# Kernel tuning notes

Hardware: AMD Instinct MI355X
Metric: run time of the kernel (lower is better)

Reference implementation:

```python
import jax, jax.numpy as jnp
import numpy as np

S, B, HID, NH = 256, 2, 512, 8
HD = HID // NH
C = 1.0            # Poincare ball curvature c (geoopt k = -c)
SQC = C ** 0.5
EPS = 1e-15


def _artanh(x):
    return jnp.arctanh(jnp.clip(x, -1 + 1e-7, 1 - 1e-7))


def artan_k(x):
    return _artanh(SQC * x) / SQC


def tan_k(x):
    return jnp.tanh(SQC * x) / SQC


def mobius_add(x, y):
    x2 = jnp.sum(x * x, -1, keepdims=True)
    y2 = jnp.sum(y * y, -1, keepdims=True)
    xy = jnp.sum(x * y, -1, keepdims=True)
    num = (1 + 2 * C * xy + C * y2) * x + (1 - C * x2) * y
    den = 1 + 2 * C * xy + C * C * x2 * y2
    return num / jnp.maximum(den, EPS)


def mobius_matvec(W, x):
    x_norm = jnp.maximum(jnp.linalg.norm(x, axis=-1, keepdims=True), EPS)
    mx = x @ W.T
    mx_norm = jnp.maximum(jnp.linalg.norm(mx, axis=-1, keepdims=True), EPS)
    res = tan_k(mx_norm / x_norm * artan_k(x_norm)) * (mx / mx_norm)
    zero = jnp.all(mx == 0, axis=-1, keepdims=True)
    return jnp.where(zero, 0.0, res)


def projx(x):
    n = jnp.maximum(jnp.linalg.norm(x, axis=-1, keepdims=True), EPS)
    maxnorm = (1 - 4e-3) / SQC  # float32 eps in geoopt
    return jnp.where(n > maxnorm, x / n * maxnorm, x)


def expmap0(u):
    n = jnp.maximum(jnp.linalg.norm(u, axis=-1, keepdims=True), EPS)
    return tan_k(n) * u / n


def logmap0(y):
    n = jnp.maximum(jnp.linalg.norm(y, axis=-1, keepdims=True), EPS)
    return artan_k(n) * y / n


def mobius_scalar_mul(r, x):
    n = jnp.maximum(jnp.linalg.norm(x, axis=-1, keepdims=True), EPS)
    return tan_k(r * artan_k(n)) * x / n


def manifold_linear(W, b, x):
    return projx(mobius_add(mobius_matvec(W, x), b))


def setup_inputs() -> dict:
    key = jax.random.key(0)
    ks = jax.random.split(key, 7)
    q = jax.random.normal(ks[0], (S, B, HID), jnp.float32) * 0.02
    w = lambda k: jax.random.normal(k, (HID, HID), jnp.float32) * 0.02
    bias = lambda k: jax.random.normal(k, (HID,), jnp.float32) * 0.01
    return {"query": q,
            "Wq": w(ks[1]), "bq": bias(ks[2]),
            "Wk": w(ks[3]), "bk": bias(ks[4]),
            "Wv": w(ks[5]), "bv": bias(ks[6])}


def reference(query, Wq, bq, Wk, bk, Wv, bv):
    x = jnp.transpose(query, (1, 0, 2))  # [B,S,HID], key=value=query
    Bn, Sn, _ = x.shape
    q = manifold_linear(Wq, bq, x)
    k = manifold_linear(Wk, bk, x)
    v = manifold_linear(Wv, bv, x)
    # faithful to torch .view(-1, H, S, D): plain memory reshape (not transpose)
    ql = expmap0(logmap0(q).reshape(Bn, NH, Sn, HD))
    kl = expmap0(logmap0(k).reshape(Bn, NH, Sn, HD))
    vl = expmap0(logmap0(v).reshape(Bn, NH, Sn, HD))
    # pairwise mobius_add(-q, k) -> [B,H,Q,N,D]; torch norm(p=-2) over D (faithful)
    diff = mobius_add(-ql[:, :, :, None, :], kl[:, :, None, :, :])
    t1 = jnp.sum(jnp.maximum(diff * diff, 1e-30) ** -1.0, axis=-1) ** -0.5
    scores = jnp.clip(-2.0 * artan_k(t1), -1e10, 1e10)
    probs = jax.nn.sigmoid(scores)  # [B,H,Q,N]; dropout p=0 -> identity
    # weighted gyro-midpoint over N (geoopt _weighted_midpoint, reducedim=[-1])
    gamma = 2.0 / jnp.maximum(1.0 - C * jnp.sum(vl * vl, -1), EPS)  # [B,H,N]
    denom = jnp.einsum('bhqn,bhn->bhq', probs, gamma - 1.0)
    sgn = jnp.where(denom >= 0, 1.0, -1.0)
    denom = sgn * jnp.maximum(jnp.abs(denom), 1e-10)
    nom = jnp.einsum('bhqn,bhnd->bhqd', probs, gamma[..., None] * vl)
    ctx = mobius_scalar_mul(0.5, nom / denom[..., None])  # [B,H,Q,D]
    ctx = jnp.transpose(ctx, (0, 2, 1, 3))  # [B,Q,H,D]
    ctx = expmap0(logmap0(ctx).reshape(Bn, Sn, HID))
    return jnp.transpose(ctx, (1, 0, 2)), probs
```

## Files before the change

### kernel.cpp

```cpp
#include <hip/hip_runtime.h>
#include <math.h>

constexpr int S_   = 256;
constexpr int B_   = 2;
constexpr int HID_ = 512;
constexpr int NH_  = 8;
constexpr int HD_  = 64;
constexpr int BSH  = B_ * S_ * HID_;

typedef unsigned short u16;
typedef short s16x8 __attribute__((ext_vector_type(8)));
typedef float f32x4 __attribute__((ext_vector_type(4)));

__device__ __forceinline__ float artanh_c(float x) {
    x = fminf(fmaxf(x, -0.9999999f), 0.9999999f);
    return 0.5f * __logf((1.f + x) / (1.f - x));
}

__device__ __forceinline__ float wsum64(float v) {
    #pragma unroll
    for (int o = 1; o < 64; o <<= 1) v += __shfl_xor(v, o, 64);
    return v;
}

__device__ __forceinline__ float block_sum_256(float v, float* red) {
    const int t = threadIdx.x;
    __syncthreads();
    red[t] = v;
    __syncthreads();
    #pragma unroll
    for (int sft = 128; sft > 0; sft >>= 1) {
        if (t < sft) red[t] += red[t + sft];
        __syncthreads();
    }
    return red[0];
}

__device__ __forceinline__ void split8(const float* v, s16x8& hi, s16x8& lo) {
    #pragma unroll
    for (int j = 0; j < 8; ++j) {
        const unsigned u = __float_as_uint(v[j]);
        const float hf = __uint_as_float(u & 0xFFFF0000u);
        hi[j] = (short)(u >> 16);
        lo[j] = (short)(__float_as_uint(v[j] - hf) >> 16);
    }
}

__global__ __launch_bounds__(256) void gemm3_fused_kernel(
    const float* __restrict__ query,
    const float* __restrict__ Wq, const float* __restrict__ Wk,
    const float* __restrict__ Wv, float* __restrict__ ws_mx)
{
    const int tid = threadIdx.x;
    const int rt = blockIdx.x >> 3;
    const int ct = blockIdx.x & 7;
    const int which = (rt * 32) >> 9;
    const int rloc  = (rt * 32) & 511;
    const float* __restrict__ W = (which == 0) ? Wq : (which == 1) ? Wk : Wv;

    __shared__ __align__(16) u16 sA[2][2][32 * 64];
    __shared__ __align__(16) u16 sB[2][2][64 * 64];

    const int ra = tid >> 3, sa = tid & 7;
    const int rb = tid >> 2, hb = (tid & 3) * 2;
    const int axrow = rloc + ra;
    const float* gA = query + (size_t)((axrow & 255) * 2 + (axrow >> 8)) * HID_ + sa * 8;
    const float* gB = W + (size_t)(ct * 64 + rb) * HID_ + hb * 8;
    const int wA  = ra * 64 + ((sa ^ (ra & 7)) * 8);
    const int wB0 = rb * 64 + ((hb ^ (rb & 7)) * 8);
    const int wB1 = rb * 64 + (((hb + 1) ^ (rb & 7)) * 8);

    const int lane = tid & 63, wv = tid >> 6;
    const int fr = lane & 15, fs = lane >> 4;
    const int aB0 = fr * 64,        ax0 = fr & 7;
    const int aB1 = (16 + fr) * 64, ax1 = (16 + fr) & 7;
    const int bB  = (wv * 16 + fr) * 64, bx = (wv * 16 + fr) & 7;

    float a8[8], b16[16];
    f32x4 acc[2] = {(f32x4){0.f,0.f,0.f,0.f}, (f32x4){0.f,0.f,0.f,0.f}};

#define G3_LOAD(c)  do { \
        const int k0 = (c) * 64; \
        *(float4*)&a8[0]  = *(const float4*)(gA + k0); \
        *(float4*)&a8[4]  = *(const float4*)(gA + k0 + 4); \
        *(float4*)&b16[0] = *(const float4*)(gB + k0); \
        *(float4*)&b16[4] = *(const float4*)(gB + k0 + 4); \
        *(float4*)&b16[8] = *(const float4*)(gB + k0 + 8); \
        *(float4*)&b16[12]= *(const float4*)(gB + k0 + 12); \
    } while (0)

#define G3_WRITE(b) do { \
        s16x8 h_, l_; \
        split8(a8, h_, l_); \
        *(s16x8*)&sA[b][0][wA] = h_;  *(s16x8*)&sA[b][1][wA] = l_; \
        split8(&b16[0], h_, l_); \
        *(s16x8*)&sB[b][0][wB0] = h_; *(s16x8*)&sB[b][1][wB0] = l_; \
        split8(&b16[8], h_, l_); \
        *(s16x8*)&sB[b][0][wB1] = h_; *(s16x8*)&sB[b][1][wB1] = l_; \
    } while (0)

    G3_LOAD(0);
    G3_WRITE(0);

    for (int c = 0; c < 8; ++c) {
        const int p = c & 1;
        __syncthreads();
        if (c < 7) G3_LOAD(c + 1);
        #pragma unroll
        for (int h = 0; h < 2; ++h) {
            const int sl = h * 4 + fs;
            s16x8 ah0 = *(const s16x8*)&sA[p][0][aB0 + ((sl ^ ax0) * 8)];
            s16x8 al0 = *(const s16x8*)&sA[p][1][aB0 + ((sl ^ ax0) * 8)];
            s16x8 ah1 = *(const s16x8*)&sA[p][0][aB1 + ((sl ^ ax1) * 8)];
            s16x8 al1 = *(const s16x8*)&sA[p][1][aB1 + ((sl ^ ax1) * 8)];
            s16x8 bh  = *(const s16x8*)&sB[p][0][bB  + ((sl ^ bx)  * 8)];
            s16x8 bl  = *(const s16x8*)&sB[p][1][bB  + ((sl ^ bx)  * 8)];
            acc[0] = __builtin_amdgcn_mfma_f32_16x16x32_bf16(ah0, bh, acc[0], 0, 0, 0);
            acc[0] = __builtin_amdgcn_mfma_f32_16x16x32_bf16(ah0, bl, acc[0], 0, 0, 0);
            acc[0] = __builtin_amdgcn_mfma_f32_16x16x32_bf16(al0, bh, acc[0], 0, 0, 0);
            acc[1] = __builtin_amdgcn_mfma_f32_16x16x32_bf16(ah1, bh, acc[1], 0, 0, 0);
            acc[1] = __builtin_amdgcn_mfma_f32_16x16x32_bf16(ah1, bl, acc[1], 0, 0, 0);
            acc[1] = __builtin_amdgcn_mfma_f32_16x16x32_bf16(al1, bh, acc[1], 0, 0, 0);
        }
        if (c < 7) G3_WRITE((c + 1) & 1);
    }
#undef G3_LOAD
#undef G3_WRITE

    #pragma unroll
    for (int i = 0; i < 2; ++i)
        #pragma unroll
        for (int q = 0; q < 4; ++q)
            ws_mx[(size_t)(rt * 32 + i * 16 + fs * 4 + q) * HID_ + ct * 64 + wv * 16 + fr]
                = acc[i][q];
}

__global__ __launch_bounds__(256) void mobius_rows_kernel(
    const float* __restrict__ query,
    const float* __restrict__ bq, const float* __restrict__ bk,
    const float* __restrict__ bv,
    float* __restrict__ ws_qkv, float* __restrict__ ws_gamma)
{
    const int lane = threadIdx.x & 63;
    const int wv   = threadIdx.x >> 6;
    const int row  = blockIdx.x * 4 + wv;
    const int which = row >> 9;
    const int rr    = row & 511;
    const float* __restrict__ bias = (which == 0) ? bq : (which == 1) ? bk : bv;
    float* mrow = ws_qkv + (size_t)row * HID_;
    const float* xrow = query + (size_t)((rr & 255) * 2 + (rr >> 8)) * HID_;

    float m[8], x[8], bb[8];
    *(float4*)&m[0]  = ((const float4*)mrow)[lane * 2];
    *(float4*)&m[4]  = ((const float4*)mrow)[lane * 2 + 1];
    *(float4*)&x[0]  = ((const float4*)xrow)[lane * 2];
    *(float4*)&x[4]  = ((const float4*)xrow)[lane * 2 + 1];
    *(float4*)&bb[0] = ((const float4*)bias)[lane * 2];
    *(float4*)&bb[4] = ((const float4*)bias)[lane * 2 + 1];

    float x2p = 0.f, m2p = 0.f, b2p = 0.f;
    #pragma unroll
    for (int j = 0; j < 8; ++j) {
        x2p = fmaf(x[j], x[j], x2p);
        m2p = fmaf(m[j], m[j], m2p);
        b2p = fmaf(bb[j], bb[j], b2p);
    }
    const float x2s = wsum64(x2p);
    const float mn2 = wsum64(m2p);
    const float b2s = wsum64(b2p);
    const float xn = fmaxf(sqrtf(x2s), 1e-15f);
    const float mn = fmaxf(sqrtf(mn2), 1e-15f);
    const float fac = tanhf(mn / xn * artanh_c(xn)) / mn;
    float r[8];
    float r2p = 0.f, ryp = 0.f;
    #pragma unroll
    for (int j = 0; j < 8; ++j) {
        r[j] = fac * m[j];
        r2p = fmaf(r[j], r[j], r2p);
        ryp = fmaf(r[j], bb[j], ryp);
    }
    const float r2s = wsum64(r2p);
    const float ry  = wsum64(ryp);
    const float a_c = 1.f + 2.f * ry + b2s;
    const float b_c = 1.f - r2s;
    const float den = 1.f + 2.f * ry + r2s * b2s;
    const float inv_den = 1.f / fmaxf(den, 1e-15f);
    float h[8];
    float h2p = 0.f;
    #pragma unroll
    for (int j = 0; j < 8; ++j) {
        h[j] = (a_c * r[j] + b_c * bb[j]) * inv_den;
        h2p = fmaf(h[j], h[j], h2p);
    }
    const float h2s = wsum64(h2p);
    float hn = fmaxf(sqrtf(h2s), 1e-15f);
    float pf = 1.f;
    if (hn > 0.996f) { pf = 0.996f / hn; hn = 0.996f; }
    const float lf = artanh_c(hn) / hn * pf;
    float l[8];
    float l2p = 0.f;
    #pragma unroll
    for (int j = 0; j < 8; ++j) {
        l[j] = lf * h[j];
        l2p = fmaf(l[j], l[j], l2p);
    }
    float cs = l2p;
    cs += __shfl_xor(cs, 1, 64);
    cs += __shfl_xor(cs, 2, 64);
    cs += __shfl_xor(cs, 4, 64);
    const float cn = fmaxf(sqrtf(cs), 1e-15f);
    const float th = tanhf(cn);
    const float sc = th / cn;
    float o[8];
    #pragma unroll
    for (int j = 0; j < 8; ++j) o[j] = sc * l[j];
    ((float4*)mrow)[lane * 2]     = *(float4*)&o[0];
    ((float4*)mrow)[lane * 2 + 1] = *(float4*)&o[4];
    if (which == 2 && (lane & 7) == 0) {
        const int j = lane >> 3;
        ws_gamma[(size_t)rr * NH_ + j] = 2.f / fmaxf(1.f - th * th, 1e-15f);
    }
}

__global__ __launch_bounds__(256) void attn_kernel(
    const float* __restrict__ ws_qkv, const float* __restrict__ gamma,
    float* __restrict__ probs, float* __restrict__ lc)
{
    const int tid = threadIdx.x;
    const int bh  = blockIdx.x >> 5;
    const int q0  = (blockIdx.x & 31) * 8;
    const float* __restrict__ ql = ws_qkv + (size_t)bh * (S_ * HD_);
    const float* __restrict__ kl = ws_qkv + (size_t)BSH + (size_t)bh * (S_ * HD_);
    const float* __restrict__ vl = ws_qkv + (size_t)2 * BSH + (size_t)bh * (S_ * HD_);

    __shared__ __align__(16) float kS[128 * 64];
    __shared__ __align__(16) float qS[8 * 64];
    __shared__ __align__(16) float pS[8 * 256];
    __shared__ float gS[S_];
    __shared__ float k2S[128];
    __shared__ float nomP[4][8][64];
    __shared__ float dnS[8];

    gS[tid] = gamma[(size_t)bh * S_ + tid];
    if (tid < 128) ((float4*)qS)[tid] = ((const float4*)(ql + (size_t)q0 * 64))[tid];
    __syncthreads();

    const int q_l = tid >> 5;
    const int n_i = tid & 31;
    float qv[64];
    #pragma unroll
    for (int c = 0; c < 16; ++c)
        *(float4*)&qv[c * 4] = *(const float4*)&qS[q_l * 64 + c * 4];
    float q2 = 0.f;
    #pragma unroll
    for (int d = 0; d < 64; ++d) q2 = fmaf(qv[d], qv[d], q2);
    const float b_c = 1.f - q2;
    float* __restrict__ prow = probs + ((size_t)(bh * S_ + q0 + q_l)) * S_;

    const int c4 = tid & 15;
    const int nb = tid >> 4;
    float sp = 0.f, spg = 0.f;

    for (int half = 0; half < 2; ++half) {
        __syncthreads();
        #pragma unroll
        for (int jj = 0; jj < 8; ++jj) {
            const int n = nb + 16 * jj;
            const float4 v = *(const float4*)(kl + ((size_t)(half * 128 + n)) * 64 + c4 * 4);
            *(float4*)&kS[n * 64 + ((c4 ^ (n & 15)) * 4)] = v;
            float pk = fmaf(v.x, v.x, fmaf(v.y, v.y, fmaf(v.z, v.z, v.w * v.w)));
            pk += __shfl_xor(pk, 1, 64);
            pk += __shfl_xor(pk, 2, 64);
            pk += __shfl_xor(pk, 4, 64);
            pk += __shfl_xor(pk, 8, 64);
            if (c4 == 0) k2S[n] = pk;
        }
        __syncthreads();
        #pragma unroll
        for (int j = 0; j < 4; ++j) {
            const int n = n_i + 32 * j;
            float kv[64];
            #pragma unroll
            for (int c = 0; c < 16; ++c)
                *(float4*)&kv[c * 4] = *(const float4*)&kS[n * 64 + ((c ^ (n & 15)) * 4)];
            float s = 0.f;
            #pragma unroll
            for (int d = 0; d < 64; ++d) s = fmaf(qv[d], kv[d], s);
            const float k2  = k2S[n];
            const float a_c = 1.f - 2.f * s + k2;
            const float den = fmaxf(fmaf(q2, k2, 1.f - 2.f * s), 1e-15f);
            const float ra  = __builtin_amdgcn_rcpf(a_c);
            const float r_c = b_c * ra;
            const float scale = den * den * ra * ra;
            const float c2  = 1e-30f * scale;
            float invsum = 0.f;
            #pragma unroll
            for (int d = 0; d < 64; ++d) {
                const float w = fmaf(r_c, kv[d], -qv[d]);
                invsum += __builtin_amdgcn_rcpf(fmaf(w, w, c2));
            }
            const float t1 = __builtin_amdgcn_rsqf(scale * invsum);
            const float p = 0.5f - 0.5f * fminf(t1, 0.9999999f);
            const int gn = half * 128 + n;
            prow[gn] = p;
            const float g = gS[gn];
            pS[q_l * 256 + gn] = p * g;
            sp += p; spg += p * g;
        }
    }
    #pragma unroll
    for (int o = 1; o < 32; o <<= 1) {
        sp  += __shfl_xor(sp, o, 64);
        spg += __shfl_xor(spg, o, 64);
    }
    if ((tid & 31) == 0) dnS[q_l] = spg - sp;
    __syncthreads();

    const int w = tid >> 6, d = tid & 63;
    float acc[8] = {};
    const float* __restrict__ vbase = vl + (size_t)(w * 64) * 64;
    #pragma unroll 4
    for (int i4 = 0; i4 < 16; ++i4) {
        float vv[4];
        #pragma unroll
        for (int j2 = 0; j2 < 4; ++j2) vv[j2] = vbase[(size_t)(i4 * 4 + j2) * 64 + d];
        #pragma unroll
        for (int qq = 0; qq < 8; ++qq) {
            const float4 pq = *(const float4*)&pS[qq * 256 + w * 64 + i4 * 4];
            acc[qq] = fmaf(pq.x, vv[0], acc[qq]);
            acc[qq] = fmaf(pq.y, vv[1], acc[qq]);
            acc[qq] = fmaf(pq.z, vv[2], acc[qq]);
            acc[qq] = fmaf(pq.w, vv[3], acc[qq]);
        }
    }
    #pragma unroll
    for (int qq = 0; qq < 8; ++qq) nomP[w][qq][d] = acc[qq];
    __syncthreads();

    #pragma unroll
    for (int t = 0; t < 2; ++t) {
        const int qq = (tid >> 6) + 4 * t;
        const float nom = nomP[0][qq][d] + nomP[1][qq][d] + nomP[2][qq][d] + nomP[3][qq][d];
        const float dd = dnS[qq];
        const float adn = fmaxf(fabsf(dd), 1e-10f);
        const float sden = (dd >= 0.f) ? adn : -adn;
        const float m = nom / sden;
        const float ss = wsum64(m * m);
        const float nn = fmaxf(sqrtf(ss), 1e-15f);
        const float s1 = tanhf(0.5f * artanh_c(nn));
        const float res = s1 * m / nn;
        const float nres = fmaxf(s1, 1e-15f);
        lc[((size_t)(bh * S_ + q0 + qq)) * HD_ + d] = (artanh_c(nres) / nres) * res;
    }
}

__global__ __launch_bounds__(256) void outproj_kernel(
    const float* __restrict__ lc, float* __restrict__ out0)
{
    const int t = threadIdx.x;
    const int s = blockIdx.x & (S_ - 1);
    const int b = blockIdx.x >> 8;
    __shared__ float red[256];
    const int h0 = t >> 6, d0 = t & 63;
    const int e1 = t + 256;
    const int h1 = e1 >> 6, d1 = e1 & 63;
    const float v0 = lc[(((size_t)(b * NH_ + h0)) * S_ + s) * HD_ + d0];
    const float v1 = lc[(((size_t)(b * NH_ + h1)) * S_ + s) * HD_ + d1];
    const float ss = block_sum_256(v0 * v0 + v1 * v1, red);
    const float nn = fmaxf(sqrtf(ss), 1e-15f);
    const float f = tanhf(nn) / nn;
    float* orow = out0 + ((size_t)(s * B_ + b)) * HID_;
    orow[t] = f * v0;
    orow[t + 256] = f * v1;
}

extern "C" void kernel_launch(void* const* d_in, const int* in_sizes, int n_in,
                              void* d_out, int out_size, void* d_ws, size_t ws_size,
                              hipStream_t stream) {
    (void)in_sizes; (void)n_in; (void)out_size; (void)ws_size;
    const float* query = (const float*)d_in[0];
    const float* Wq = (const float*)d_in[1];
    const float* bq = (const float*)d_in[2];
    const float* Wk = (const float*)d_in[3];
    const float* bk = (const float*)d_in[4];
    const float* Wv = (const float*)d_in[5];
    const float* bv = (const float*)d_in[6];

    float* out0  = (float*)d_out;
    float* probs = out0 + (size_t)S_ * B_ * HID_;

    float* ws       = (float*)d_ws;
    float* ws_qkv   = ws;
    float* ws_gamma = ws + (size_t)3 * BSH;
    float* ws_lc    = ws + (size_t)3 * BSH + 4096;

    gemm3_fused_kernel<<<dim3(384), dim3(256), 0, stream>>>(query, Wq, Wk, Wv, ws_qkv);
    mobius_rows_kernel<<<dim3(384), dim3(256), 0, stream>>>(query, bq, bk, bv, ws_qkv, ws_gamma);
    attn_kernel<<<dim3(512), dim3(256), 0, stream>>>(ws_qkv, ws_gamma, probs, ws_lc);
    outproj_kernel<<<dim3(B_ * S_), dim3(256), 0, stream>>>(ws_lc, out0);
}
```

Measured before the change: 108.8 us.

## Split attention head dimension across two half-waves with 512-thread blocks

Doubles the attention kernel's block to 512 threads and has each query's 64 lanes split the 64-wide head dimension into two 32-element halves, combining partial dot products and reciprocal sums with a cross-half shuffle. This halves per-thread register arrays (qv/kv) so more waves can be resident and the latency-bound per-pair work is spread over more threads. The PV accumulation is re-partitioned over 8 warps of 32 keys each, and the nomP reduction grows to 8 partials. It adds extra shuffles and leaves half the lanes idle for the store and probability-accumulation step.

```diff
diff --git a/kernel.cpp b/kernel.cpp
--- a/kernel.cpp
+++ b/kernel.cpp
@@ -7,6 +7,7 @@
 constexpr int NH_  = 8;
 constexpr int HD_  = 64;
 constexpr int BSH  = B_ * S_ * HID_;
+
 
 typedef unsigned short u16;
 typedef short s16x8 __attribute__((ext_vector_type(8)));
@@ -222,7 +223,7 @@
     }
 }
 
-__global__ __launch_bounds__(256) void attn_kernel(
+__global__ __launch_bounds__(512, 4) void attn_kernel(
     const float* __restrict__ ws_qkv, const float* __restrict__ gamma,
     float* __restrict__ probs, float* __restrict__ lc)
 {
@@ -238,22 +239,27 @@
     __shared__ __align__(16) float pS[8 * 256];
     __shared__ float gS[S_];
     __shared__ float k2S[128];
-    __shared__ float nomP[4][8][64];
+    __shared__ float nomP[8][8][64];
     __shared__ float dnS[8];
 
-    gS[tid] = gamma[(size_t)bh * S_ + tid];
+    if (tid < 256) gS[tid] = gamma[(size_t)bh * S_ + tid];
     if (tid < 128) ((float4*)qS)[tid] = ((const float4*)(ql + (size_t)q0 * 64))[tid];
     __syncthreads();
 
-    const int q_l = tid >> 5;
-    const int n_i = tid & 31;
-    float qv[64];
-    #pragma unroll
-    for (int c = 0; c < 16; ++c)
-        *(float4*)&qv[c * 4] = *(const float4*)&qS[q_l * 64 + c * 4];
-    float q2 = 0.f;
-    #pragma unroll
-    for (int d = 0; d < 64; ++d) q2 = fmaf(qv[d], qv[d], q2);
+    const int lane = tid & 63;
+    const int q_l  = tid >> 6;
+    const int n_i  = lane & 31;
+    const int dh   = lane >> 5;
+    const int d0   = dh * 32;
+
+    float qv[32];
+    #pragma unroll
+    for (int c = 0; c < 8; ++c)
+        *(float4*)&qv[c * 4] = *(const float4*)&qS[q_l * 64 + d0 + c * 4];
+    float q2p = 0.f;
+    #pragma unroll
+    for (int d = 0; d < 32; ++d) q2p = fmaf(qv[d], qv[d], q2p);
+    const float q2 = q2p + __shfl_xor(q2p, 32, 64);
     const float b_c = 1.f - q2;
     float* __restrict__ prow = probs + ((size_t)(bh * S_ + q0 + q_l)) * S_;
 
@@ -264,8 +270,8 @@
     for (int half = 0; half < 2; ++half) {
         __syncthreads();
         #pragma unroll
-        for (int jj = 0; jj < 8; ++jj) {
-            const int n = nb + 16 * jj;
+        for (int jj = 0; jj < 4; ++jj) {
+            const int n = nb + 32 * jj;
             const float4 v = *(const float4*)(kl + ((size_t)(half * 128 + n)) * 64 + c4 * 4);
             *(float4*)&kS[n * 64 + ((c4 ^ (n & 15)) * 4)] = v;
             float pk = fmaf(v.x, v.x, fmaf(v.y, v.y, fmaf(v.z, v.z, v.w * v.w)));
@@ -279,13 +285,20 @@
         #pragma unroll
         for (int j = 0; j < 4; ++j) {
             const int n = n_i + 32 * j;
-            float kv[64];
+            float kv[32];
             #pragma unroll
-            for (int c = 0; c < 16; ++c)
-                *(float4*)&kv[c * 4] = *(const float4*)&kS[n * 64 + ((c ^ (n & 15)) * 4)];
-            float s = 0.f;
+            for (int c = 0; c < 8; ++c) {
+                const int sl = dh * 8 + c;
+                *(float4*)&kv[c * 4] = *(const float4*)&kS[n * 64 + ((sl ^ (n & 15)) * 4)];
+            }
+            float s0 = 0.f, s1 = 0.f;
             #pragma unroll
-            for (int d = 0; d < 64; ++d) s = fmaf(qv[d], kv[d], s);
+            for (int d = 0; d < 32; d += 2) {
+                s0 = fmaf(qv[d],     kv[d],     s0);
+                s1 = fmaf(qv[d + 1], kv[d + 1], s1);
+            }
+            float s = s0 + s1;
+            s += __shfl_xor(s, 32, 64);
             const float k2  = k2S[n];
             const float a_c = 1.f - 2.f * s + k2;
             const float den = fmaxf(fmaf(q2, k2, 1.f - 2.f * s), 1e-15f);
@@ -293,40 +306,43 @@
             const float r_c = b_c * ra;
             const float scale = den * den * ra * ra;
             const float c2  = 1e-30f * scale;
-            float invsum = 0.f;
+            float is0 = 0.f, is1 = 0.f;
             #pragma unroll
-            for (int d = 0; d < 64; ++d) {
-                const float w = fmaf(r_c, kv[d], -qv[d]);
-                invsum += __builtin_amdgcn_rcpf(fmaf(w, w, c2));
+            for (int d = 0; d < 32; d += 2) {
+                const float w0 = fmaf(r_c, kv[d],     -qv[d]);
+                const float w1 = fmaf(r_c, kv[d + 1], -qv[d + 1]);
+                is0 += __builtin_amdgcn_rcpf(fmaf(w0, w0, c2));
+                is1 += __builtin_amdgcn_rcpf(fmaf(w1, w1, c2));
             }
+            float invsum = is0 + is1;
+            invsum += __shfl_xor(invsum, 32, 64);
             const float t1 = __builtin_amdgcn_rsqf(scale * invsum);
             const float p = 0.5f - 0.5f * fminf(t1, 0.9999999f);
             const int gn = half * 128 + n;
-            prow[gn] = p;
-            const float g = gS[gn];
-            pS[q_l * 256 + gn] = p * g;
-            sp += p; spg += p * g;
+            if (dh == 0) {
+                prow[gn] = p;
+                const float g = gS[gn];
+                pS[q_l * 256 + gn] = p * g;
+                sp += p; spg += p * g;
+            }
         }
     }
-    #pragma unroll
-    for (int o = 1; o < 32; o <<= 1) {
-        sp  += __shfl_xor(sp, o, 64);
-        spg += __shfl_xor(spg, o, 64);
-    }
-    if ((tid & 31) == 0) dnS[q_l] = spg - sp;
+    sp  = wsum64(sp);
+    spg = wsum64(spg);
+    if (lane == 0) dnS[q_l] = spg - sp;
     __syncthreads();
 
-    const int w = tid >> 6, d = tid & 63;
+    const int w = q_l, d = lane;
     float acc[8] = {};
-    const float* __restrict__ vbase = vl + (size_t)(w * 64) * 64;
-    #pragma unroll 4
-    for (int i4 = 0; i4 < 16; ++i4) {
+    const float* __restrict__ vbase = vl + (size_t)(w * 32) * 64;
+    #pragma unroll
+    for (int i4 = 0; i4 < 8; ++i4) {
         float vv[4];
         #pragma unroll
         for (int j2 = 0; j2 < 4; ++j2) vv[j2] = vbase[(size_t)(i4 * 4 + j2) * 64 + d];
         #pragma unroll
         for (int qq = 0; qq < 8; ++qq) {
-            const float4 pq = *(const float4*)&pS[qq * 256 + w * 64 + i4 * 4];
+            const float4 pq = *(const float4*)&pS[qq * 256 + w * 32 + i4 * 4];
             acc[qq] = fmaf(pq.x, vv[0], acc[qq]);
             acc[qq] = fmaf(pq.y, vv[1], acc[qq]);
             acc[qq] = fmaf(pq.z, vv[2], acc[qq]);
@@ -337,10 +353,11 @@
     for (int qq = 0; qq < 8; ++qq) nomP[w][qq][d] = acc[qq];
     __syncthreads();
 
-    #pragma unroll
-    for (int t = 0; t < 2; ++t) {
-        const int qq = (tid >> 6) + 4 * t;
-        const float nom = nomP[0][qq][d] + nomP[1][qq][d] + nomP[2][qq][d] + nomP[3][qq][d];
+    {
+        const int qq = q_l;
+        float nom = 0.f;
+        #pragma unroll
+        for (int w2 = 0; w2 < 8; ++w2) nom += nomP[w2][qq][d];
         const float dd = dnS[qq];
         const float adn = fmaxf(fabsf(dd), 1e-10f);
         const float sden = (dd >= 0.f) ? adn : -adn;
@@ -396,6 +413,6 @@
 
     gemm3_fused_kernel<<<dim3(384), dim3(256), 0, stream>>>(query, Wq, Wk, Wv, ws_qkv);
     mobius_rows_kernel<<<dim3(384), dim3(256), 0, stream>>>(query, bq, bk, bv, ws_qkv, ws_gamma);
-    attn_kernel<<<dim3(512), dim3(256), 0, stream>>>(ws_qkv, ws_gamma, probs, ws_lc);
+    attn_kernel<<<dim3(512), dim3(512), 0, stream>>>(ws_qkv, ws_gamma, probs, ws_lc);
     outproj_kernel<<<dim3(B_ * S_), dim3(256), 0, stream>>>(ws_lc, out0);
 }
```

Measured after the change: 106.6 us. 2.0% less time.

## Restructure attention: one key per thread, 4 queries per block, more blocks

Applied to the files above, without the earlier changes.

The attention kernel now assigns one key row per thread, held in registers and read directly from global memory, and loops over 4 queries per block. This replaces the LDS-staged, swizzled key tiles with 8 queries per block. The grid doubles to 1024 blocks and the block index is remapped so the head varies fastest. Query rows are read from global memory in the inner loop, and the dot-product and reciprocal-sum accumulations are split four ways for ILP. Gamma is now applied to V inside the nominator loop, and the denominator reduction is moved to after scoring. Keys are now re-read from global or L2 by every block, and 64-float key arrays per thread raise register pressure.

```diff
diff --git a/kernel.cpp b/kernel.cpp
--- a/kernel.cpp
+++ b/kernel.cpp
@@ -7,6 +7,7 @@
 constexpr int NH_  = 8;
 constexpr int HD_  = 64;
 constexpr int BSH  = B_ * S_ * HID_;
+
 
 typedef unsigned short u16;
 typedef short s16x8 __attribute__((ext_vector_type(8)));
@@ -227,120 +228,123 @@
     float* __restrict__ probs, float* __restrict__ lc)
 {
     const int tid = threadIdx.x;
-    const int bh  = blockIdx.x >> 5;
-    const int q0  = (blockIdx.x & 31) * 8;
+    const int bh  = blockIdx.x & 15;
+    const int q0  = (blockIdx.x >> 4) * 4;
     const float* __restrict__ ql = ws_qkv + (size_t)bh * (S_ * HD_);
     const float* __restrict__ kl = ws_qkv + (size_t)BSH + (size_t)bh * (S_ * HD_);
     const float* __restrict__ vl = ws_qkv + (size_t)2 * BSH + (size_t)bh * (S_ * HD_);
 
-    __shared__ __align__(16) float kS[128 * 64];
-    __shared__ __align__(16) float qS[8 * 64];
-    __shared__ __align__(16) float pS[8 * 256];
+    __shared__ float pP[4][256];
     __shared__ float gS[S_];
-    __shared__ float k2S[128];
-    __shared__ float nomP[4][8][64];
-    __shared__ float dnS[8];
+    __shared__ float nomP[4][4][64];
+    __shared__ float q2S[4];
+    __shared__ float dnS[4];
 
     gS[tid] = gamma[(size_t)bh * S_ + tid];
-    if (tid < 128) ((float4*)qS)[tid] = ((const float4*)(ql + (size_t)q0 * 64))[tid];
+
+    const int n = tid;
+    float kv[64];
+    #pragma unroll
+    for (int c = 0; c < 16; ++c)
+        *(float4*)&kv[c * 4] = *(const float4*)(kl + (size_t)n * 64 + c * 4);
+    float k2a = 0.f, k2b = 0.f;
+    #pragma unroll
+    for (int d = 0; d < 64; d += 2) {
+        k2a = fmaf(kv[d],     kv[d],     k2a);
+        k2b = fmaf(kv[d + 1], kv[d + 1], k2b);
+    }
+    const float k2 = k2a + k2b;
+
+    if (tid < 4) {
+        const float* qr = ql + (size_t)(q0 + tid) * 64;
+        float s = 0.f;
+        #pragma unroll
+        for (int d = 0; d < 64; ++d) s = fmaf(qr[d], qr[d], s);
+        q2S[tid] = s;
+    }
     __syncthreads();
 
-    const int q_l = tid >> 5;
-    const int n_i = tid & 31;
-    float qv[64];
-    #pragma unroll
-    for (int c = 0; c < 16; ++c)
-        *(float4*)&qv[c * 4] = *(const float4*)&qS[q_l * 64 + c * 4];
-    float q2 = 0.f;
-    #pragma unroll
-    for (int d = 0; d < 64; ++d) q2 = fmaf(qv[d], qv[d], q2);
-    const float b_c = 1.f - q2;
-    float* __restrict__ prow = probs + ((size_t)(bh * S_ + q0 + q_l)) * S_;
-
-    const int c4 = tid & 15;
-    const int nb = tid >> 4;
-    float sp = 0.f, spg = 0.f;
-
-    for (int half = 0; half < 2; ++half) {
-        __syncthreads();
-        #pragma unroll
-        for (int jj = 0; jj < 8; ++jj) {
-            const int n = nb + 16 * jj;
-            const float4 v = *(const float4*)(kl + ((size_t)(half * 128 + n)) * 64 + c4 * 4);
-            *(float4*)&kS[n * 64 + ((c4 ^ (n & 15)) * 4)] = v;
-            float pk = fmaf(v.x, v.x, fmaf(v.y, v.y, fmaf(v.z, v.z, v.w * v.w)));
-            pk += __shfl_xor(pk, 1, 64);
-            pk += __shfl_xor(pk, 2, 64);
-            pk += __shfl_xor(pk, 4, 64);
-            pk += __shfl_xor(pk, 8, 64);
-            if (c4 == 0) k2S[n] = pk;
+    #pragma unroll
+    for (int q = 0; q < 4; ++q) {
+        const float* __restrict__ qrow = ql + (size_t)(q0 + q) * 64;
+        const float q2  = q2S[q];
+        const float b_c = 1.f - q2;
+        float s0 = 0.f, s1 = 0.f, s2 = 0.f, s3 = 0.f;
+        #pragma unroll
+        for (int d = 0; d < 64; d += 4) {
+            s0 = fmaf(kv[d],     qrow[d],     s0);
+            s1 = fmaf(kv[d + 1], qrow[d + 1], s1);
+            s2 = fmaf(kv[d + 2], qrow[d + 2], s2);
+            s3 = fmaf(kv[d + 3], qrow[d + 3], s3);
         }
-        __syncthreads();
-        #pragma unroll
-        for (int j = 0; j < 4; ++j) {
-            const int n = n_i + 32 * j;
-            float kv[64];
-            #pragma unroll
-            for (int c = 0; c < 16; ++c)
-                *(float4*)&kv[c * 4] = *(const float4*)&kS[n * 64 + ((c ^ (n & 15)) * 4)];
-            float s = 0.f;
-            #pragma unroll
-            for (int d = 0; d < 64; ++d) s = fmaf(qv[d], kv[d], s);
-            const float k2  = k2S[n];
-            const float a_c = 1.f - 2.f * s + k2;
-            const float den = fmaxf(fmaf(q2, k2, 1.f - 2.f * s), 1e-15f);
-            const float ra  = __builtin_amdgcn_rcpf(a_c);
-            const float r_c = b_c * ra;
-            const float scale = den * den * ra * ra;
-            const float c2  = 1e-30f * scale;
-            float invsum = 0.f;
-            #pragma unroll
-            for (int d = 0; d < 64; ++d) {
-                const float w = fmaf(r_c, kv[d], -qv[d]);
-                invsum += __builtin_amdgcn_rcpf(fmaf(w, w, c2));
-            }
-            const float t1 = __builtin_amdgcn_rsqf(scale * invsum);
-            const float p = 0.5f - 0.5f * fminf(t1, 0.9999999f);
-            const int gn = half * 128 + n;
-            prow[gn] = p;
-            const float g = gS[gn];
-            pS[q_l * 256 + gn] = p * g;
-            sp += p; spg += p * g;
+        const float s = (s0 + s1) + (s2 + s3);
+        const float a_c = 1.f - 2.f * s + k2;
+        const float den = fmaxf(fmaf(q2, k2, 1.f - 2.f * s), 1e-15f);
+        const float ra  = __builtin_amdgcn_rcpf(a_c);
+        const float r_c = b_c * ra;
+        const float scale = den * den * ra * ra;
+        const float c2  = 1e-30f * scale;
+        float i0 = 0.f, i1 = 0.f, i2 = 0.f, i3 = 0.f;
+        #pragma unroll
+        for (int d = 0; d < 64; d += 4) {
+            const float w0 = fmaf(r_c, kv[d],     -qrow[d]);
+            const float w1 = fmaf(r_c, kv[d + 1], -qrow[d + 1]);
+            const float w2 = fmaf(r_c, kv[d + 2], -qrow[d + 2]);
+            const float w3 = fmaf(r_c, kv[d + 3], -qrow[d + 3]);
+            i0 += __builtin_amdgcn_rcpf(fmaf(w0, w0, c2));
+            i1 += __builtin_amdgcn_rcpf(fmaf(w1, w1, c2));
+            i2 += __builtin_amdgcn_rcpf(fmaf(w2, w2, c2));
+            i3 += __builtin_amdgcn_rcpf(fmaf(w3, w3, c2));
         }
-    }
-    #pragma unroll
-    for (int o = 1; o < 32; o <<= 1) {
-        sp  += __shfl_xor(sp, o, 64);
-        spg += __shfl_xor(spg, o, 64);
-    }
-    if ((tid & 31) == 0) dnS[q_l] = spg - sp;
+        const float invsum = (i0 + i1) + (i2 + i3);
+        const float t1 = __builtin_amdgcn_rsqf(scale * invsum);
+        const float p = 0.5f - 0.5f * fminf(t1, 0.9999999f);
+        probs[((size_t)(bh * S_ + q0 + q)) * S_ + n] = p;
+        pP[q][n] = p;
+    }
     __syncthreads();
 
     const int w = tid >> 6, d = tid & 63;
-    float acc[8] = {};
+    {
+        float sp = 0.f, spg = 0.f;
+        #pragma unroll
+        for (int m = 0; m < 4; ++m) {
+            const float p = pP[w][d + 64 * m];
+            const float g = gS[d + 64 * m];
+            sp += p; spg = fmaf(p, g, spg);
+        }
+        sp = wsum64(sp);
+        spg = wsum64(spg);
+        if (d == 0) dnS[w] = spg - sp;
+    }
+
+    float acc[4] = {};
     const float* __restrict__ vbase = vl + (size_t)(w * 64) * 64;
     #pragma unroll 4
     for (int i4 = 0; i4 < 16; ++i4) {
-        float vv[4];
-        #pragma unroll
-        for (int j2 = 0; j2 < 4; ++j2) vv[j2] = vbase[(size_t)(i4 * 4 + j2) * 64 + d];
-        #pragma unroll
-        for (int qq = 0; qq < 8; ++qq) {
-            const float4 pq = *(const float4*)&pS[qq * 256 + w * 64 + i4 * 4];
-            acc[qq] = fmaf(pq.x, vv[0], acc[qq]);
-            acc[qq] = fmaf(pq.y, vv[1], acc[qq]);
-            acc[qq] = fmaf(pq.z, vv[2], acc[qq]);
-            acc[qq] = fmaf(pq.w, vv[3], acc[qq]);
+        float gv[4];
+        const float4 g4 = *(const float4*)&gS[w * 64 + i4 * 4];
+        #pragma unroll
+        for (int j2 = 0; j2 < 4; ++j2)
+            gv[j2] = ((const float*)&g4)[j2] * vbase[(size_t)(i4 * 4 + j2) * 64 + d];
+        #pragma unroll
+        for (int qq = 0; qq < 4; ++qq) {
+            const float4 pq = *(const float4*)&pP[qq][w * 64 + i4 * 4];
+            acc[qq] = fmaf(pq.x, gv[0], acc[qq]);
+            acc[qq] = fmaf(pq.y, gv[1], acc[qq]);
+            acc[qq] = fmaf(pq.z, gv[2], acc[qq]);
+            acc[qq] = fmaf(pq.w, gv[3], acc[qq]);
         }
     }
     #pragma unroll
-    for (int qq = 0; qq < 8; ++qq) nomP[w][qq][d] = acc[qq];
+    for (int qq = 0; qq < 4; ++qq) nomP[w][qq][d] = acc[qq];
     __syncthreads();
 
-    #pragma unroll
-    for (int t = 0; t < 2; ++t) {
-        const int qq = (tid >> 6) + 4 * t;
-        const float nom = nomP[0][qq][d] + nomP[1][qq][d] + nomP[2][qq][d] + nomP[3][qq][d];
+    {
+        const int qq = w;
+        float nom = 0.f;
+        #pragma unroll
+        for (int w2 = 0; w2 < 4; ++w2) nom += nomP[w2][qq][d];
         const float dd = dnS[qq];
         const float adn = fmaxf(fabsf(dd), 1e-10f);
         const float sden = (dd >= 0.f) ? adn : -adn;
@@ -396,6 +400,6 @@
 
     gemm3_fused_kernel<<<dim3(384), dim3(256), 0, stream>>>(query, Wq, Wk, Wv, ws_qkv);
     mobius_rows_kernel<<<dim3(384), dim3(256), 0, stream>>>(query, bq, bk, bv, ws_qkv, ws_gamma);
-    attn_kernel<<<dim3(512), dim3(256), 0, stream>>>(ws_qkv, ws_gamma, probs, ws_lc);
+    attn_kernel<<<dim3(1024), dim3(256), 0, stream>>>(ws_qkv, ws_gamma, probs, ws_lc);
     outproj_kernel<<<dim3(B_ * S_), dim3(256), 0, stream>>>(ws_lc, out0);
 }
```

Result: slower. 116.0 us (+6.5%).
